# Kernel optimization log

Measured on AMD Instinct MI355X. Metric: run time of the kernel, lower is better.

Reference implementation:

```python
import jax, jax.numpy as jnp
import numpy as np

CTX = 64       # context_size_samples
HOP = 128      # stft hop
CUT = 129      # filter_length//2 + 1


def conv1d(x, w, b, stride, pad):
    # x: [B, Cin, L], w: [Cout, Cin, K]
    out = jax.lax.conv_general_dilated(
        x, w, window_strides=(stride,), padding=[(pad, pad)],
        dimension_numbers=("NCH", "OIH", "NCH"))
    return out + b[None, :, None]


def setup_inputs() -> dict:
    key = jax.random.key(0)
    ks = jax.random.split(key, 16)
    B = 32768
    s = 0.05  # small init scale to avoid gate/sigmoid saturation
    inp = {
        "x": jax.random.normal(ks[0], (B, 512), jnp.float32),
        "h0": jnp.zeros((B, 128), jnp.float32),
        "c0": jnp.zeros((B, 128), jnp.float32),
        "basis": jax.random.normal(ks[1], (258, 1, 256), jnp.float32) * s,
        "w1": jax.random.normal(ks[2], (128, 129, 3), jnp.float32) * s,
        "b1": jax.random.normal(ks[3], (128,), jnp.float32) * s,
        "w2": jax.random.normal(ks[4], (64, 128, 3), jnp.float32) * s,
        "b2": jax.random.normal(ks[5], (64,), jnp.float32) * s,
        "w3": jax.random.normal(ks[6], (64, 64, 3), jnp.float32) * s,
        "b3": jax.random.normal(ks[7], (64,), jnp.float32) * s,
        "w4": jax.random.normal(ks[8], (128, 64, 3), jnp.float32) * s,
        "b4": jax.random.normal(ks[9], (128,), jnp.float32) * s,
        "w_ih": jax.random.normal(ks[10], (512, 128), jnp.float32) * s,
        "w_hh": jax.random.normal(ks[11], (512, 128), jnp.float32) * s,
        "b_ih": jax.random.normal(ks[12], (512,), jnp.float32) * s,
        "b_hh": jax.random.normal(ks[13], (512,), jnp.float32) * s,
        "dec_w": jax.random.normal(ks[14], (1, 128, 1), jnp.float32) * s,
        "dec_b": jax.random.normal(ks[15], (1,), jnp.float32) * s,
    }
    return inp


def reference(x, h0, c0, basis, w1, b1, w2, b2, w3, b3, w4, b4,
              w_ih, w_hh, b_ih, b_hh, dec_w, dec_b):
    B = x.shape[0]
    # prepend zero context, reflect-pad by 64 (ConvSTFT)
    xc = jnp.concatenate([jnp.zeros((B, CTX), x.dtype), x], axis=1)  # [B,576]
    xp = jnp.pad(xc, ((0, 0), (64, 64)), mode="reflect")[:, None, :]  # [B,1,704]
    ft = jax.lax.conv_general_dilated(
        xp, basis, window_strides=(HOP,), padding=[(0, 0)],
        dimension_numbers=("NCH", "OIH", "NCH"))  # [B,258,4]
    real, imag = ft[:, :CUT, :], ft[:, CUT:, :]
    mag = jnp.sqrt(real * real + imag * imag)  # [B,129,4]
    # encoder: 4 conv+relu blocks
    e = jax.nn.relu(conv1d(mag, w1, b1, 1, 1))   # [B,128,4]
    e = jax.nn.relu(conv1d(e, w2, b2, 2, 1))     # [B,64,2]
    e = jax.nn.relu(conv1d(e, w3, b3, 2, 1))     # [B,64,1]
    e = jax.nn.relu(conv1d(e, w4, b4, 1, 1))     # [B,128,1]
    dec_in = e[:, :, 0]  # [B,128]
    # LSTM cell (gate order i,f,g,o as in the slicing)
    gates = dec_in @ w_ih.T + b_ih + h0 @ w_hh.T + b_hh  # [B,512]
    i, f, g, o = jnp.split(gates, 4, axis=1)
    c1 = jax.nn.sigmoid(f) * c0 + jax.nn.sigmoid(i) * jnp.tanh(g)
    h1 = jax.nn.sigmoid(o) * jnp.tanh(c1)
    # decoder: (eval-mode dropout = identity) -> ReLU -> 1x1 conv -> sigmoid
    out = jax.nn.sigmoid(jax.nn.relu(h1) @ dec_w[0, :, 0] + dec_b[0])  # [B]
    # mean over length-1 dim + squeeze is identity here
    return out, h1, c1
```

## Files before the change

### kernel.cpp

```cpp
#include <hip/hip_runtime.h>

typedef _Float16 f16;
typedef _Float16 f16x8 __attribute__((ext_vector_type(8)));
typedef _Float16 f16x4 __attribute__((ext_vector_type(4)));
typedef float f32x4 __attribute__((ext_vector_type(4)));

#define MFMA16(a, b, c) __builtin_amdgcn_mfma_f32_16x16x32_f16((a), (b), (c), 0, 0, 0)

#define BATCH 32768

#define OFF_XP      ((size_t)0)
#define OFF_MAGP    ((size_t)46137344)
#define OFF_BF      (OFF_MAGP + 54525952)
#define OFF_W1      (OFF_BF + 139264)
#define OFF_W2      (OFF_W1 + 106496)
#define OFF_W3      (OFF_W2 + 49152)
#define OFF_W4      (OFF_W3 + 24576)
#define OFF_WG      (OFF_W4 + 16384)

__device__ __forceinline__ float sigmoid_(float x) { return 1.f / (1.f + __expf(-x)); }

__global__ __launch_bounds__(256) void prep_kernel(
    const float* __restrict__ x, const float* __restrict__ basis,
    const float* __restrict__ w1, const float* __restrict__ w2,
    const float* __restrict__ w3, const float* __restrict__ w4,
    const float* __restrict__ w_ih, const float* __restrict__ w_hh,
    f16* __restrict__ xp, f16* __restrict__ magP,
    f16* __restrict__ Bf3, f16* __restrict__ W1i, f16* __restrict__ W2,
    f16* __restrict__ W3, f16* __restrict__ W4, f16* __restrict__ Wg) {
  int blk = blockIdx.x;
  int tid = threadIdx.x;
  if (blk < 1024) {
    int b0 = blk * 32;
    for (int idx = tid; idx < 32 * 176; idx += 256) {
      int bl = idx / 176, g = idx - bl * 176;
      int b = b0 + bl;
      f16x4 o;
      if (g < 32) {
        float v0 = (g == 0) ? x[(size_t)b * 512] : 0.f;
        o = (f16x4){(f16)v0, (f16)0.f, (f16)0.f, (f16)0.f};
      } else if (g < 160) {
        const float4 v = *(const float4*)(x + (size_t)b * 512 + 4 * g - 128);
        o = (f16x4){(f16)v.x, (f16)v.y, (f16)v.z, (f16)v.w};
      } else {
        int j0 = 4 * g;
        const float* xb = x + (size_t)b * 512;
        o = (f16x4){(f16)xb[1150 - j0], (f16)xb[1149 - j0], (f16)xb[1148 - j0],
                    (f16)xb[1147 - j0]};
      }
      *(f16x4*)(xp + (size_t)b * 704 + 4 * g) = o;
    }
    f16x8 z8 = {};
    for (int idx = tid; idx < 32 * 36; idx += 256) {
      int bl = idx / 36, g = idx - bl * 36;
      int off = (g < 17) ? g * 8 : 680 + (g - 17) * 8;
      *(f16x8*)(magP + (size_t)(b0 + bl) * 832 + off) = z8;
    }
  } else {
    int t = (blk - 1024) * 256 + tid;
    for (int idx = t; idx < 8 * 17 * 512; idx += 16384) {
      int jj = idx & 7;
      int lane = (idx >> 3) & 63;
      int rest = idx >> 9;
      int tt = rest % 17, kb = rest / 17;
      int n = tt * 16 + (lane & 15);
      int k = kb * 32 + (lane >> 4) * 8 + jj;
      Bf3[idx] = (f16)((n < 258) ? basis[n * 256 + k] : 0.f);
    }
    for (int idx = t; idx < 13 * 128 * 32; idx += 16384) {
      int kb = idx / 4096, rest = idx - kb * 4096;
      int n = rest >> 5, kk = rest & 31;
      int k = kb * 32 + kk;
      int tap = k / 136, i = k - tap * 136;
      float v = (tap < 3 && i < 129) ? w1[(n * 129 + i) * 3 + tap] : 0.f;
      W1i[idx] = (f16)v;
    }
    for (int idx = t; idx < 64 * 384; idx += 16384) {
      int n = idx / 384, k = idx - n * 384;
      int tap = k >> 7, i = k & 127;
      W2[idx] = (f16)w2[(n * 128 + i) * 3 + tap];
    }
    for (int idx = t; idx < 64 * 192; idx += 16384) {
      int n = idx / 192, k = idx - n * 192;
      int tap = k >> 6, i = k & 63;
      W3[idx] = (f16)w3[(n * 64 + i) * 3 + tap];
    }
    for (int idx = t; idx < 128 * 64; idx += 16384) {
      int n = idx >> 6, i = idx & 63;
      W4[idx] = (f16)w4[(n * 64 + i) * 3 + 1];
    }
    for (int idx = t; idx < 512 * 256; idx += 16384) {
      int n = idx >> 8, k = idx & 255;
      Wg[idx] = (f16)((k < 128) ? w_ih[n * 128 + k] : w_hh[n * 128 + (k - 128)]);
    }
  }
}

__global__ __launch_bounds__(256) void stft_kernel(
    const f16* __restrict__ xp, const f16* __restrict__ Bf3,
    f16* __restrict__ magP) {
  __shared__ __align__(16) f16 Bslab[2][17 * 512];
  __shared__ float imPatch[4][64];
  int tid = threadIdx.x;
  int lane = tid & 63, wv = tid >> 6;
  int l15 = lane & 15, quad = lane >> 4;
  int m0 = blockIdx.x * 64;

  int t0 = 2 * wv, t1 = 2 * wv + 1, t2 = 2 * wv + 8, t3 = 2 * wv + 9;

  f32x4 zero4 = {0.f, 0.f, 0.f, 0.f};
  f32x4 acc[4][4];
  f32x4 acc4[4];
#pragma unroll
  for (int s = 0; s < 4; s++)
#pragma unroll
    for (int mt = 0; mt < 4; mt++) acc[s][mt] = zero4;
#pragma unroll
  for (int mt = 0; mt < 4; mt++) acc4[mt] = zero4;

  const f16* aptr[4];
#pragma unroll
  for (int mt = 0; mt < 4; mt++) {
    int m = m0 + mt * 16 + l15;
    int b = m >> 2, t = m & 3;
    aptr[mt] = xp + (size_t)b * 704 + t * 128 + quad * 8;
  }

  f16x8 stg[5];
#pragma unroll
  for (int i = 0; i < 5; i++) {
    int j = wv + 4 * i;
    if (j < 17) stg[i] = *(const f16x8*)(Bf3 + (size_t)j * 512 + lane * 8);
  }
#pragma unroll
  for (int i = 0; i < 5; i++) {
    int j = wv + 4 * i;
    if (j < 17) *(f16x8*)&Bslab[0][j * 512 + lane * 8] = stg[i];
  }

  for (int kb = 0; kb < 8; kb++) {
    __syncthreads();
    int cur = kb & 1;
    if (kb < 7) {
#pragma unroll
      for (int i = 0; i < 5; i++) {
        int j = wv + 4 * i;
        if (j < 17)
          stg[i] = *(const f16x8*)(Bf3 + ((size_t)(kb + 1) * 17 + j) * 512 +
                                   lane * 8);
      }
    }
    f16x8 a[4];
#pragma unroll
    for (int mt = 0; mt < 4; mt++) a[mt] = *(const f16x8*)(aptr[mt] + kb * 32);
    {
      f16x8 b0f = *(const f16x8*)&Bslab[cur][t0 * 512 + lane * 8];
      f16x8 b1f = *(const f16x8*)&Bslab[cur][t1 * 512 + lane * 8];
      f16x8 b2f = *(const f16x8*)&Bslab[cur][t2 * 512 + lane * 8];
      f16x8 b3f = *(const f16x8*)&Bslab[cur][t3 * 512 + lane * 8];
#pragma unroll
      for (int mt = 0; mt < 4; mt++) {
        acc[0][mt] = MFMA16(a[mt], b0f, acc[0][mt]);
        acc[1][mt] = MFMA16(a[mt], b1f, acc[1][mt]);
        acc[2][mt] = MFMA16(a[mt], b2f, acc[2][mt]);
        acc[3][mt] = MFMA16(a[mt], b3f, acc[3][mt]);
      }
      if (wv == 0) {
        f16x8 b4f = *(const f16x8*)&Bslab[cur][16 * 512 + lane * 8];
#pragma unroll
        for (int mt = 0; mt < 4; mt++) acc4[mt] = MFMA16(a[mt], b4f, acc4[mt]);
      }
    }
    if (kb < 7) {
#pragma unroll
      for (int i = 0; i < 5; i++) {
        int j = wv + 4 * i;
        if (j < 17) *(f16x8*)&Bslab[cur ^ 1][j * 512 + lane * 8] = stg[i];
      }
    }
  }

  __syncthreads();
  {
    int dst = (wv == 0) ? 3 : (wv - 1);
    if (l15 == 0) {
#pragma unroll
      for (int mt = 0; mt < 4; mt++)
#pragma unroll
        for (int r = 0; r < 4; r++) {
          int row = mt * 16 + quad * 4 + r;
          imPatch[dst][row] = (wv == 0) ? acc4[mt][r] : acc[2][mt][r];
        }
    }
  }
  __syncthreads();

#pragma unroll
  for (int mt = 0; mt < 4; mt++)
#pragma unroll
    for (int r = 0; r < 4; r++) {
      int row = mt * 16 + quad * 4 + r;
      int m = m0 + row;
      int b = m >> 2, t = m & 3;
      f16* orow = magP + (size_t)b * 832 + (t + 1) * 136;
      {
        float re = acc[0][mt][r];
        float imA = __shfl(acc[2][mt][r], (quad << 4) | ((l15 + 1) & 15), 64);
        float imB = __shfl(acc[3][mt][r], quad << 4, 64);
        float im = (l15 == 15) ? imB : imA;
        orow[32 * wv + l15] = (f16)sqrtf(re * re + im * im);
      }
      {
        float re = acc[1][mt][r];
        float imA = __shfl(acc[3][mt][r], (quad << 4) | ((l15 + 1) & 15), 64);
        float im = (l15 == 15) ? imPatch[wv][row] : imA;
        orow[32 * wv + 16 + l15] = (f16)sqrtf(re * re + im * im);
      }
      if (wv == 0) {
        float re = acc[2][mt][r];
        float im = __shfl(acc4[mt][r], (quad << 4) | 1, 64);
        if (l15 == 0) orow[128] = (f16)sqrtf(re * re + im * im);
      }
    }
}

__global__ __launch_bounds__(256) void tail_kernel(
    const f16* __restrict__ magP, const f16* __restrict__ W1i,
    const float* __restrict__ b1, const f16* __restrict__ W2,
    const float* __restrict__ b2, const f16* __restrict__ W3,
    const float* __restrict__ b3, const f16* __restrict__ W4,
    const float* __restrict__ b4, const f16* __restrict__ Wg,
    const float* __restrict__ b_ih, const float* __restrict__ b_hh,
    const float* __restrict__ h0, const float* __restrict__ c0,
    const float* __restrict__ dec_w, const float* __restrict__ dec_b,
    float* __restrict__ out) {
  __shared__ __align__(16) char smem[54272];
  f16* SF = (f16*)smem;
  float* part = (float*)(smem + 21504);
#define E1(bl, s, c) ((bl) * 648 + (s) * 128 + (c))
#define E2(bl, s, c) (20736 + (bl) * 200 + (s) * 64 + (c))
#define E3(bl, c) ((bl) * 72 + (c))
#define E4(bl, k) (2304 + (bl) * 264 + (k))

  int tid = threadIdx.x;
  int lane = tid & 63, wv = tid >> 6;
  int l15 = lane & 15, quad = lane >> 4;
  int b0 = blockIdx.x * 32;
  f32x4 zero4 = {0.f, 0.f, 0.f, 0.f};

  {
    f16x8 z8 = {};
    for (int idx = tid; idx < 512; idx += 256) {
      int bl = idx >> 4, g = idx & 15;
      *(f16x8*)&SF[E1(bl, 0, g * 8)] = z8;
    }
    for (int idx = tid; idx < 256; idx += 256) {
      int bl = idx >> 3, g = idx & 7;
      *(f16x8*)&SF[E2(bl, 0, g * 8)] = z8;
    }
  }

  {
    f32x4 acc1[8][2];
#pragma unroll
    for (int mt = 0; mt < 8; mt++)
#pragma unroll
      for (int nt = 0; nt < 2; nt++) acc1[mt][nt] = zero4;
    const f16* aptr[8];
#pragma unroll
    for (int mt = 0; mt < 8; mt++) {
      int row = mt * 16 + l15;
      int b = b0 + (row >> 2), p = row & 3;
      aptr[mt] = magP + (size_t)b * 832 + p * 136 + quad * 8;
    }
    const f16* bbase = W1i + ((2 * wv) * 16 + l15) * 32 + quad * 8;
    for (int kb = 0; kb < 13; kb++) {
      f16x8 a[8];
#pragma unroll
      for (int mt = 0; mt < 8; mt++) a[mt] = *(const f16x8*)(aptr[mt] + kb * 32);
      f16x8 bf0 = *(const f16x8*)(bbase + kb * 4096);
      f16x8 bf1 = *(const f16x8*)(bbase + kb * 4096 + 512);
#pragma unroll
      for (int mt = 0; mt < 8; mt++) {
        acc1[mt][0] = MFMA16(a[mt], bf0, acc1[mt][0]);
        acc1[mt][1] = MFMA16(a[mt], bf1, acc1[mt][1]);
      }
    }
    float bias[2];
#pragma unroll
    for (int nt = 0; nt < 2; nt++) bias[nt] = b1[(2 * wv + nt) * 16 + l15];
#pragma unroll
    for (int mt = 0; mt < 8; mt++)
#pragma unroll
      for (int r = 0; r < 4; r++) {
        int row = mt * 16 + quad * 4 + r;
        int bl = row >> 2, p = row & 3;
#pragma unroll
        for (int nt = 0; nt < 2; nt++) {
          int c = (2 * wv + nt) * 16 + l15;
          SF[E1(bl, p + 1, c)] = (f16)fmaxf(acc1[mt][nt][r] + bias[nt], 0.f);
        }
      }
  }
  __syncthreads();

  {
    int wr = wv & 1, wc = wv >> 1;
    f32x4 acc2[2][2];
#pragma unroll
    for (int mt = 0; mt < 2; mt++)
#pragma unroll
      for (int nt = 0; nt < 2; nt++) acc2[mt][nt] = zero4;
    int abase[2];
#pragma unroll
    for (int mt = 0; mt < 2; mt++) {
      int row2 = wr * 32 + mt * 16 + l15;
      int bl = row2 >> 1, p2 = row2 & 1;
      abase[mt] = E1(bl, 2 * p2, quad * 8);
    }
    const f16* bbase = W2 + (size_t)(wc * 32 + l15) * 384 + quad * 8;
    for (int kb = 0; kb < 12; kb++) {
      f16x8 a0 = *(const f16x8*)&SF[abase[0] + kb * 32];
      f16x8 a1 = *(const f16x8*)&SF[abase[1] + kb * 32];
      f16x8 bf0 = *(const f16x8*)(bbase + kb * 32);
      f16x8 bf1 = *(const f16x8*)(bbase + 16 * 384 + kb * 32);
      acc2[0][0] = MFMA16(a0, bf0, acc2[0][0]);
      acc2[1][0] = MFMA16(a1, bf0, acc2[1][0]);
      acc2[0][1] = MFMA16(a0, bf1, acc2[0][1]);
      acc2[1][1] = MFMA16(a1, bf1, acc2[1][1]);
    }
    float bias[2];
#pragma unroll
    for (int nt = 0; nt < 2; nt++) bias[nt] = b2[wc * 32 + nt * 16 + l15];
#pragma unroll
    for (int mt = 0; mt < 2; mt++)
#pragma unroll
      for (int r = 0; r < 4; r++) {
        int row2 = wr * 32 + mt * 16 + quad * 4 + r;
        int bl = row2 >> 1, p2 = row2 & 1;
#pragma unroll
        for (int nt = 0; nt < 2; nt++) {
          int c = wc * 32 + nt * 16 + l15;
          SF[E2(bl, p2 + 1, c)] = (f16)fmaxf(acc2[mt][nt][r] + bias[nt], 0.f);
        }
      }
  }
  __syncthreads();

  {
    for (int idx = tid; idx < 1024; idx += 256) {
      int bl = idx >> 5, jg = idx & 31;
      const float4 v = *(const float4*)(h0 + (size_t)(b0 + bl) * 128 + jg * 4);
      f16x4 o = {(f16)v.x, (f16)v.y, (f16)v.z, (f16)v.w};
      *(f16x4*)&SF[E4(bl, 128 + jg * 4)] = o;
    }
    f32x4 acc3[2];
#pragma unroll
    for (int mt = 0; mt < 2; mt++) acc3[mt] = zero4;
    const f16* bbase = W3 + (size_t)(wv * 16 + l15) * 192 + quad * 8;
    for (int kb = 0; kb < 6; kb++) {
      f16x8 a0 = *(const f16x8*)&SF[E2(l15, 0, 0) + kb * 32 + quad * 8];
      f16x8 a1 = *(const f16x8*)&SF[E2(16 + l15, 0, 0) + kb * 32 + quad * 8];
      f16x8 bf = *(const f16x8*)(bbase + kb * 32);
      acc3[0] = MFMA16(a0, bf, acc3[0]);
      acc3[1] = MFMA16(a1, bf, acc3[1]);
    }
    float bias = b3[wv * 16 + l15];
#pragma unroll
    for (int mt = 0; mt < 2; mt++)
#pragma unroll
      for (int r = 0; r < 4; r++) {
        int bl = mt * 16 + quad * 4 + r;
        SF[E3(bl, wv * 16 + l15)] = (f16)fmaxf(acc3[mt][r] + bias, 0.f);
      }
  }
  __syncthreads();

  {
    f32x4 acc4[2][2];
#pragma unroll
    for (int mt = 0; mt < 2; mt++)
#pragma unroll
      for (int nt = 0; nt < 2; nt++) acc4[mt][nt] = zero4;
    const f16* bbase = W4 + (size_t)(wv * 32 + l15) * 64 + quad * 8;
    for (int kb = 0; kb < 2; kb++) {
      f16x8 a0 = *(const f16x8*)&SF[E3(l15, kb * 32 + quad * 8)];
      f16x8 a1 = *(const f16x8*)&SF[E3(16 + l15, kb * 32 + quad * 8)];
      f16x8 bf0 = *(const f16x8*)(bbase + kb * 32);
      f16x8 bf1 = *(const f16x8*)(bbase + 16 * 64 + kb * 32);
      acc4[0][0] = MFMA16(a0, bf0, acc4[0][0]);
      acc4[1][0] = MFMA16(a1, bf0, acc4[1][0]);
      acc4[0][1] = MFMA16(a0, bf1, acc4[0][1]);
      acc4[1][1] = MFMA16(a1, bf1, acc4[1][1]);
    }
    float bias[2];
#pragma unroll
    for (int nt = 0; nt < 2; nt++) bias[nt] = b4[wv * 32 + nt * 16 + l15];
#pragma unroll
    for (int mt = 0; mt < 2; mt++)
#pragma unroll
      for (int r = 0; r < 4; r++) {
        int bl = mt * 16 + quad * 4 + r;
#pragma unroll
        for (int nt = 0; nt < 2; nt++) {
          int c = wv * 32 + nt * 16 + l15;
          SF[E4(bl, c)] = (f16)fmaxf(acc4[mt][nt][r] + bias[nt], 0.f);
        }
      }
  }
  __syncthreads();

  {
    f32x4 accg[8][2];
#pragma unroll
    for (int j = 0; j < 8; j++)
#pragma unroll
      for (int mt = 0; mt < 2; mt++) accg[j][mt] = zero4;
    const f16* bptrs[8];
#pragma unroll
    for (int q = 0; q < 4; q++)
#pragma unroll
      for (int u = 0; u < 2; u++)
        bptrs[q * 2 + u] =
            Wg + (size_t)(q * 128 + wv * 32 + u * 16 + l15) * 256 + quad * 8;
    for (int kb = 0; kb < 8; kb++) {
      f16x8 a0 = *(const f16x8*)&SF[E4(l15, kb * 32 + quad * 8)];
      f16x8 a1 = *(const f16x8*)&SF[E4(16 + l15, kb * 32 + quad * 8)];
#pragma unroll
      for (int j = 0; j < 8; j++) {
        f16x8 bf = *(const f16x8*)(bptrs[j] + kb * 32);
        accg[j][0] = MFMA16(a0, bf, accg[j][0]);
        accg[j][1] = MFMA16(a1, bf, accg[j][1]);
      }
    }
    float bias[8], dw[2];
#pragma unroll
    for (int q = 0; q < 4; q++)
#pragma unroll
      for (int u = 0; u < 2; u++) {
        int n = q * 128 + wv * 32 + u * 16 + l15;
        bias[q * 2 + u] = b_ih[n] + b_hh[n];
      }
#pragma unroll
    for (int u = 0; u < 2; u++) dw[u] = dec_w[wv * 32 + u * 16 + l15];

    float* out_h1 = out + BATCH;
    float* out_c1 = out + BATCH + (size_t)BATCH * 128;
#pragma unroll
    for (int mt = 0; mt < 2; mt++)
#pragma unroll
      for (int r = 0; r < 4; r++) {
        int bl = mt * 16 + quad * 4 + r;
        int b = b0 + bl;
        float p = 0.f;
#pragma unroll
        for (int u = 0; u < 2; u++) {
          int c = wv * 32 + u * 16 + l15;
          float iv = accg[0 + u][mt][r] + bias[0 + u];
          float fv = accg[2 + u][mt][r] + bias[2 + u];
          float gv = accg[4 + u][mt][r] + bias[4 + u];
          float ov = accg[6 + u][mt][r] + bias[6 + u];
          float c0v = c0[(size_t)b * 128 + c];
          float c1 = sigmoid_(fv) * c0v + sigmoid_(iv) * tanhf(gv);
          float h1 = sigmoid_(ov) * tanhf(c1);
          out_h1[(size_t)b * 128 + c] = h1;
          out_c1[(size_t)b * 128 + c] = c1;
          p += fmaxf(h1, 0.f) * dw[u];
        }
        p += __shfl_xor(p, 1);
        p += __shfl_xor(p, 2);
        p += __shfl_xor(p, 4);
        p += __shfl_xor(p, 8);
        if (l15 == 0) part[wv * 32 + bl] = p;
      }
  }
  __syncthreads();
  if (tid < 32) {
    float s = part[tid] + part[32 + tid] + part[64 + tid] + part[96 + tid] +
              dec_b[0];
    out[b0 + tid] = 1.f / (1.f + __expf(-s));
  }
#undef E1
#undef E2
#undef E3
#undef E4
}

extern "C" void kernel_launch(void* const* d_in, const int* in_sizes, int n_in,
                              void* d_out, int out_size, void* d_ws,
                              size_t ws_size, hipStream_t stream) {
  const float* x = (const float*)d_in[0];
  const float* h0 = (const float*)d_in[1];
  const float* c0 = (const float*)d_in[2];
  const float* basis = (const float*)d_in[3];
  const float* w1 = (const float*)d_in[4];
  const float* b1 = (const float*)d_in[5];
  const float* w2 = (const float*)d_in[6];
  const float* b2 = (const float*)d_in[7];
  const float* w3 = (const float*)d_in[8];
  const float* b3 = (const float*)d_in[9];
  const float* w4 = (const float*)d_in[10];
  const float* b4 = (const float*)d_in[11];
  const float* w_ih = (const float*)d_in[12];
  const float* w_hh = (const float*)d_in[13];
  const float* b_ih = (const float*)d_in[14];
  const float* b_hh = (const float*)d_in[15];
  const float* dec_w = (const float*)d_in[16];
  const float* dec_b = (const float*)d_in[17];

  char* ws = (char*)d_ws;
  f16* xp = (f16*)(ws + OFF_XP);
  f16* magP = (f16*)(ws + OFF_MAGP);
  f16* Bf3 = (f16*)(ws + OFF_BF);
  f16* W1i = (f16*)(ws + OFF_W1);
  f16* W2 = (f16*)(ws + OFF_W2);
  f16* W3 = (f16*)(ws + OFF_W3);
  f16* W4 = (f16*)(ws + OFF_W4);
  f16* Wg = (f16*)(ws + OFF_WG);

  prep_kernel<<<1088, 256, 0, stream>>>(x, basis, w1, w2, w3, w4, w_ih, w_hh,
                                        xp, magP, Bf3, W1i, W2, W3, W4, Wg);
  stft_kernel<<<2048, 256, 0, stream>>>(xp, Bf3, magP);
  tail_kernel<<<1024, 256, 0, stream>>>(magP, W1i, b1, W2, b2, W3, b3, W4, b4,
                                        Wg, b_ih, b_hh, h0, c0, dec_w, dec_b,
                                        (float*)d_out);
}
```

Before: 359.1 us.

## Fuse STFT and encoder convs into one kernel, split LSTM gates out

Padding the input, the STFT matmul, the magnitude and all four encoder conv layers now run in one kernel per 16-sample tile, with intermediates held in shared memory. This removes the global round trips through the padded-input and magnitude buffers. Only the encoder output, plus h0 written by the prep kernel, goes to a small global buffer, and a separate gates kernel runs the LSTM matmul on 64-row tiles. In exchange, the basis and conv weights are read straight from global or cache into registers rather than staged in LDS, tiles are smaller (16 rows), and the kernel uses more LDS per block.

```diff
diff --git a/kernel.cpp b/kernel.cpp
--- a/kernel.cpp
+++ b/kernel.cpp
@@ -9,9 +9,8 @@
 
 #define BATCH 32768
 
-#define OFF_XP      ((size_t)0)
-#define OFF_MAGP    ((size_t)46137344)
-#define OFF_BF      (OFF_MAGP + 54525952)
+#define OFF_GATESA  ((size_t)0)
+#define OFF_BF      (OFF_GATESA + 16777216)
 #define OFF_W1      (OFF_BF + 139264)
 #define OFF_W2      (OFF_W1 + 106496)
 #define OFF_W3      (OFF_W2 + 49152)
@@ -21,40 +20,22 @@
 __device__ __forceinline__ float sigmoid_(float x) { return 1.f / (1.f + __expf(-x)); }
 
 __global__ __launch_bounds__(256) void prep_kernel(
-    const float* __restrict__ x, const float* __restrict__ basis,
+    const float* __restrict__ h0, const float* __restrict__ basis,
     const float* __restrict__ w1, const float* __restrict__ w2,
     const float* __restrict__ w3, const float* __restrict__ w4,
     const float* __restrict__ w_ih, const float* __restrict__ w_hh,
-    f16* __restrict__ xp, f16* __restrict__ magP,
-    f16* __restrict__ Bf3, f16* __restrict__ W1i, f16* __restrict__ W2,
-    f16* __restrict__ W3, f16* __restrict__ W4, f16* __restrict__ Wg) {
+    f16* __restrict__ gatesA, f16* __restrict__ Bf3, f16* __restrict__ W1i,
+    f16* __restrict__ W2, f16* __restrict__ W3, f16* __restrict__ W4,
+    f16* __restrict__ Wg) {
   int blk = blockIdx.x;
   int tid = threadIdx.x;
   if (blk < 1024) {
     int b0 = blk * 32;
-    for (int idx = tid; idx < 32 * 176; idx += 256) {
-      int bl = idx / 176, g = idx - bl * 176;
-      int b = b0 + bl;
-      f16x4 o;
-      if (g < 32) {
-        float v0 = (g == 0) ? x[(size_t)b * 512] : 0.f;
-        o = (f16x4){(f16)v0, (f16)0.f, (f16)0.f, (f16)0.f};
-      } else if (g < 160) {
-        const float4 v = *(const float4*)(x + (size_t)b * 512 + 4 * g - 128);
-        o = (f16x4){(f16)v.x, (f16)v.y, (f16)v.z, (f16)v.w};
-      } else {
-        int j0 = 4 * g;
-        const float* xb = x + (size_t)b * 512;
-        o = (f16x4){(f16)xb[1150 - j0], (f16)xb[1149 - j0], (f16)xb[1148 - j0],
-                    (f16)xb[1147 - j0]};
-      }
-      *(f16x4*)(xp + (size_t)b * 704 + 4 * g) = o;
-    }
-    f16x8 z8 = {};
-    for (int idx = tid; idx < 32 * 36; idx += 256) {
-      int bl = idx / 36, g = idx - bl * 36;
-      int off = (g < 17) ? g * 8 : 680 + (g - 17) * 8;
-      *(f16x8*)(magP + (size_t)(b0 + bl) * 832 + off) = z8;
+    for (int idx = tid; idx < 32 * 32; idx += 256) {
+      int bl = idx >> 5, g = idx & 31;
+      const float4 v = *(const float4*)(h0 + (size_t)(b0 + bl) * 128 + g * 4);
+      f16x4 o = {(f16)v.x, (f16)v.y, (f16)v.z, (f16)v.w};
+      *(f16x4*)(gatesA + (size_t)(b0 + bl) * 256 + 128 + g * 4) = o;
     }
   } else {
     int t = (blk - 1024) * 256 + tid;
@@ -96,394 +77,362 @@
   }
 }
 
-__global__ __launch_bounds__(256) void stft_kernel(
-    const f16* __restrict__ xp, const f16* __restrict__ Bf3,
-    f16* __restrict__ magP) {
-  __shared__ __align__(16) f16 Bslab[2][17 * 512];
-  __shared__ float imPatch[4][64];
+__global__ __launch_bounds__(256, 2) void fused_kernel(
+    const float* __restrict__ x, const f16* __restrict__ Bf3,
+    const f16* __restrict__ W1i, const float* __restrict__ b1,
+    const f16* __restrict__ W2, const float* __restrict__ b2,
+    const f16* __restrict__ W3, const float* __restrict__ b3,
+    const f16* __restrict__ W4, const float* __restrict__ b4,
+    f16* __restrict__ gatesA) {
+  __shared__ __align__(16) char smem[57088];
+  f16* SF = (f16*)smem;
+  float* imPatch = (float*)(smem + 56064);
+#define XP(bl, j) ((bl)*712 + (j))
+#define E1(bl, s, c) ((bl)*648 + (s)*128 + (c))
+#define E3(bl, c) ((bl)*72 + (c))
+#define MG(bl, j) (11392 + (bl)*840 + (j))
+#define E2(bl, s, c) (24832 + (bl)*200 + (s)*64 + (c))
+
   int tid = threadIdx.x;
   int lane = tid & 63, wv = tid >> 6;
   int l15 = lane & 15, quad = lane >> 4;
-  int m0 = blockIdx.x * 64;
-
-  int t0 = 2 * wv, t1 = 2 * wv + 1, t2 = 2 * wv + 8, t3 = 2 * wv + 9;
-
+  int b0 = blockIdx.x * 16;
   f32x4 zero4 = {0.f, 0.f, 0.f, 0.f};
-  f32x4 acc[4][4];
-  f32x4 acc4[4];
-#pragma unroll
-  for (int s = 0; s < 4; s++)
-#pragma unroll
-    for (int mt = 0; mt < 4; mt++) acc[s][mt] = zero4;
-#pragma unroll
-  for (int mt = 0; mt < 4; mt++) acc4[mt] = zero4;
-
-  const f16* aptr[4];
-#pragma unroll
-  for (int mt = 0; mt < 4; mt++) {
-    int m = m0 + mt * 16 + l15;
-    int b = m >> 2, t = m & 3;
-    aptr[mt] = xp + (size_t)b * 704 + t * 128 + quad * 8;
-  }
-
-  f16x8 stg[5];
-#pragma unroll
-  for (int i = 0; i < 5; i++) {
-    int j = wv + 4 * i;
-    if (j < 17) stg[i] = *(const f16x8*)(Bf3 + (size_t)j * 512 + lane * 8);
-  }
-#pragma unroll
-  for (int i = 0; i < 5; i++) {
-    int j = wv + 4 * i;
-    if (j < 17) *(f16x8*)&Bslab[0][j * 512 + lane * 8] = stg[i];
-  }
-
-  for (int kb = 0; kb < 8; kb++) {
+
+  for (int idx = tid; idx < 16 * 176; idx += 256) {
+    int bl = idx / 176, g = idx - bl * 176;
+    int b = b0 + bl;
+    f16x4 o;
+    if (g < 32) {
+      float v0 = (g == 0) ? x[(size_t)b * 512] : 0.f;
+      o = (f16x4){(f16)v0, (f16)0.f, (f16)0.f, (f16)0.f};
+    } else if (g < 160) {
+      const float4 v = *(const float4*)(x + (size_t)b * 512 + 4 * g - 128);
+      o = (f16x4){(f16)v.x, (f16)v.y, (f16)v.z, (f16)v.w};
+    } else {
+      int j0 = 4 * g;
+      const float* xb = x + (size_t)b * 512;
+      o = (f16x4){(f16)xb[1150 - j0], (f16)xb[1149 - j0], (f16)xb[1148 - j0],
+                  (f16)xb[1147 - j0]};
+    }
+    *(f16x4*)&SF[XP(bl, 4 * g)] = o;
+  }
+  {
+    f16x8 z8 = {};
+    for (int idx = tid; idx < 16 * 105; idx += 256) {
+      int bl = idx / 105, g = idx - bl * 105;
+      *(f16x8*)&SF[MG(bl, g * 8)] = z8;
+    }
+    for (int idx = tid; idx < 16 * 8; idx += 256) {
+      int bl = idx >> 3, g = idx & 7;
+      *(f16x8*)&SF[E2(bl, 0, g * 8)] = z8;
+    }
+  }
+  __syncthreads();
+
+  {
+    int t0 = 2 * wv, t1 = t0 + 1, t2 = t0 + 8, t3 = t0 + 9;
+    f32x4 acc[4][4];
+    f32x4 acc4[4];
+#pragma unroll
+    for (int s = 0; s < 4; s++)
+#pragma unroll
+      for (int mt = 0; mt < 4; mt++) acc[s][mt] = zero4;
+#pragma unroll
+    for (int mt = 0; mt < 4; mt++) acc4[mt] = zero4;
+
+    const f16* Bl = Bf3 + lane * 8;
+    f16x8 bc0 = *(const f16x8*)(Bl + t0 * 512);
+    f16x8 bc1 = *(const f16x8*)(Bl + t1 * 512);
+    f16x8 bc2 = *(const f16x8*)(Bl + t2 * 512);
+    f16x8 bc3 = *(const f16x8*)(Bl + t3 * 512);
+    f16x8 bc4 = {};
+    if (wv == 0) bc4 = *(const f16x8*)(Bl + 16 * 512);
+
+    for (int kb = 0; kb < 8; kb++) {
+      f16x8 bn0, bn1, bn2, bn3, bn4;
+      if (kb < 7) {
+        const f16* Bn = Bl + (size_t)(kb + 1) * 17 * 512;
+        bn0 = *(const f16x8*)(Bn + t0 * 512);
+        bn1 = *(const f16x8*)(Bn + t1 * 512);
+        bn2 = *(const f16x8*)(Bn + t2 * 512);
+        bn3 = *(const f16x8*)(Bn + t3 * 512);
+        if (wv == 0) bn4 = *(const f16x8*)(Bn + 16 * 512);
+      }
+      f16x8 a[4];
+#pragma unroll
+      for (int mt = 0; mt < 4; mt++)
+        a[mt] = *(const f16x8*)&SF[XP(l15, mt * 128 + kb * 32 + quad * 8)];
+#pragma unroll
+      for (int mt = 0; mt < 4; mt++) {
+        acc[0][mt] = MFMA16(a[mt], bc0, acc[0][mt]);
+        acc[1][mt] = MFMA16(a[mt], bc1, acc[1][mt]);
+        acc[2][mt] = MFMA16(a[mt], bc2, acc[2][mt]);
+        acc[3][mt] = MFMA16(a[mt], bc3, acc[3][mt]);
+      }
+      if (wv == 0) {
+#pragma unroll
+        for (int mt = 0; mt < 4; mt++) acc4[mt] = MFMA16(a[mt], bc4, acc4[mt]);
+      }
+      if (kb < 7) {
+        bc0 = bn0; bc1 = bn1; bc2 = bn2; bc3 = bn3;
+        if (wv == 0) bc4 = bn4;
+      }
+    }
+
+    {
+      int dst = (wv == 0) ? 3 : (wv - 1);
+      if (l15 == 0) {
+#pragma unroll
+        for (int mt = 0; mt < 4; mt++)
+#pragma unroll
+          for (int r = 0; r < 4; r++) {
+            int row = mt * 16 + quad * 4 + r;
+            imPatch[dst * 64 + row] = (wv == 0) ? acc4[mt][r] : acc[2][mt][r];
+          }
+      }
+    }
     __syncthreads();
-    int cur = kb & 1;
-    if (kb < 7) {
-#pragma unroll
-      for (int i = 0; i < 5; i++) {
-        int j = wv + 4 * i;
-        if (j < 17)
-          stg[i] = *(const f16x8*)(Bf3 + ((size_t)(kb + 1) * 17 + j) * 512 +
-                                   lane * 8);
-      }
-    }
-    f16x8 a[4];
-#pragma unroll
-    for (int mt = 0; mt < 4; mt++) a[mt] = *(const f16x8*)(aptr[mt] + kb * 32);
-    {
-      f16x8 b0f = *(const f16x8*)&Bslab[cur][t0 * 512 + lane * 8];
-      f16x8 b1f = *(const f16x8*)&Bslab[cur][t1 * 512 + lane * 8];
-      f16x8 b2f = *(const f16x8*)&Bslab[cur][t2 * 512 + lane * 8];
-      f16x8 b3f = *(const f16x8*)&Bslab[cur][t3 * 512 + lane * 8];
-#pragma unroll
-      for (int mt = 0; mt < 4; mt++) {
-        acc[0][mt] = MFMA16(a[mt], b0f, acc[0][mt]);
-        acc[1][mt] = MFMA16(a[mt], b1f, acc[1][mt]);
-        acc[2][mt] = MFMA16(a[mt], b2f, acc[2][mt]);
-        acc[3][mt] = MFMA16(a[mt], b3f, acc[3][mt]);
-      }
-      if (wv == 0) {
-        f16x8 b4f = *(const f16x8*)&Bslab[cur][16 * 512 + lane * 8];
-#pragma unroll
-        for (int mt = 0; mt < 4; mt++) acc4[mt] = MFMA16(a[mt], b4f, acc4[mt]);
-      }
-    }
-    if (kb < 7) {
-#pragma unroll
-      for (int i = 0; i < 5; i++) {
-        int j = wv + 4 * i;
-        if (j < 17) *(f16x8*)&Bslab[cur ^ 1][j * 512 + lane * 8] = stg[i];
-      }
-    }
-  }
-
-  __syncthreads();
-  {
-    int dst = (wv == 0) ? 3 : (wv - 1);
-    if (l15 == 0) {
-#pragma unroll
-      for (int mt = 0; mt < 4; mt++)
-#pragma unroll
-        for (int r = 0; r < 4; r++) {
+
+#pragma unroll
+    for (int mt = 0; mt < 4; mt++)
+#pragma unroll
+      for (int r = 0; r < 4; r++) {
+        int bl = quad * 4 + r;
+        int orow = MG(bl, (mt + 1) * 136);
+        {
+          float re = acc[0][mt][r];
+          float imA = __shfl(acc[2][mt][r], (quad << 4) | ((l15 + 1) & 15), 64);
+          float imB = __shfl(acc[3][mt][r], quad << 4, 64);
+          float im = (l15 == 15) ? imB : imA;
+          SF[orow + 32 * wv + l15] = (f16)sqrtf(re * re + im * im);
+        }
+        {
+          float re = acc[1][mt][r];
+          float imA = __shfl(acc[3][mt][r], (quad << 4) | ((l15 + 1) & 15), 64);
           int row = mt * 16 + quad * 4 + r;
-          imPatch[dst][row] = (wv == 0) ? acc4[mt][r] : acc[2][mt][r];
+          float im = (l15 == 15) ? imPatch[wv * 64 + row] : imA;
+          SF[orow + 32 * wv + 16 + l15] = (f16)sqrtf(re * re + im * im);
         }
-    }
-  }
-  __syncthreads();
-
-#pragma unroll
-  for (int mt = 0; mt < 4; mt++)
+        if (wv == 0) {
+          float re = acc[2][mt][r];
+          float im = __shfl(acc4[mt][r], (quad << 4) | 1, 64);
+          if (l15 == 0) SF[orow + 128] = (f16)sqrtf(re * re + im * im);
+        }
+      }
+  }
+  __syncthreads();
+
+  {
+    f16x8 z8 = {};
+    for (int idx = tid; idx < 16 * 16; idx += 256) {
+      int bl = idx >> 4, g = idx & 15;
+      *(f16x8*)&SF[E1(bl, 0, g * 8)] = z8;
+    }
+    f32x4 acc1[4][2];
+#pragma unroll
+    for (int p = 0; p < 4; p++)
+#pragma unroll
+      for (int nt = 0; nt < 2; nt++) acc1[p][nt] = zero4;
+    const f16* bbase = W1i + ((2 * wv) * 16 + l15) * 32 + quad * 8;
+    f16x8 bc0 = *(const f16x8*)(bbase);
+    f16x8 bc1 = *(const f16x8*)(bbase + 512);
+    for (int kb = 0; kb < 13; kb++) {
+      f16x8 bn0, bn1;
+      if (kb < 12) {
+        bn0 = *(const f16x8*)(bbase + (kb + 1) * 4096);
+        bn1 = *(const f16x8*)(bbase + (kb + 1) * 4096 + 512);
+      }
+      f16x8 a[4];
+#pragma unroll
+      for (int p = 0; p < 4; p++)
+        a[p] = *(const f16x8*)&SF[MG(l15, p * 136 + kb * 32 + quad * 8)];
+#pragma unroll
+      for (int p = 0; p < 4; p++) {
+        acc1[p][0] = MFMA16(a[p], bc0, acc1[p][0]);
+        acc1[p][1] = MFMA16(a[p], bc1, acc1[p][1]);
+      }
+      if (kb < 12) { bc0 = bn0; bc1 = bn1; }
+    }
+    float bias[2];
+#pragma unroll
+    for (int nt = 0; nt < 2; nt++) bias[nt] = b1[(2 * wv + nt) * 16 + l15];
+#pragma unroll
+    for (int p = 0; p < 4; p++)
+#pragma unroll
+      for (int r = 0; r < 4; r++) {
+        int bl = quad * 4 + r;
+#pragma unroll
+        for (int nt = 0; nt < 2; nt++) {
+          int c = (2 * wv + nt) * 16 + l15;
+          SF[E1(bl, p + 1, c)] = (f16)fmaxf(acc1[p][nt][r] + bias[nt], 0.f);
+        }
+      }
+  }
+  __syncthreads();
+
+  {
+    int wr = wv & 1, wc = wv >> 1;
+    f32x4 acc2[2] = {zero4, zero4};
+    const f16* bbase = W2 + (size_t)(wc * 32 + l15) * 384 + quad * 8;
+    f16x8 bc0 = *(const f16x8*)(bbase);
+    f16x8 bc1 = *(const f16x8*)(bbase + 16 * 384);
+    for (int kb = 0; kb < 12; kb++) {
+      f16x8 bn0, bn1;
+      if (kb < 11) {
+        bn0 = *(const f16x8*)(bbase + (kb + 1) * 32);
+        bn1 = *(const f16x8*)(bbase + 16 * 384 + (kb + 1) * 32);
+      }
+      f16x8 a = *(const f16x8*)&SF[E1(l15, wr * 2, kb * 32 + quad * 8)];
+      acc2[0] = MFMA16(a, bc0, acc2[0]);
+      acc2[1] = MFMA16(a, bc1, acc2[1]);
+      if (kb < 11) { bc0 = bn0; bc1 = bn1; }
+    }
+    float bias[2] = {b2[wc * 32 + l15], b2[wc * 32 + 16 + l15]};
 #pragma unroll
     for (int r = 0; r < 4; r++) {
-      int row = mt * 16 + quad * 4 + r;
-      int m = m0 + row;
-      int b = m >> 2, t = m & 3;
-      f16* orow = magP + (size_t)b * 832 + (t + 1) * 136;
-      {
-        float re = acc[0][mt][r];
-        float imA = __shfl(acc[2][mt][r], (quad << 4) | ((l15 + 1) & 15), 64);
-        float imB = __shfl(acc[3][mt][r], quad << 4, 64);
-        float im = (l15 == 15) ? imB : imA;
-        orow[32 * wv + l15] = (f16)sqrtf(re * re + im * im);
-      }
-      {
-        float re = acc[1][mt][r];
-        float imA = __shfl(acc[3][mt][r], (quad << 4) | ((l15 + 1) & 15), 64);
-        float im = (l15 == 15) ? imPatch[wv][row] : imA;
-        orow[32 * wv + 16 + l15] = (f16)sqrtf(re * re + im * im);
-      }
-      if (wv == 0) {
-        float re = acc[2][mt][r];
-        float im = __shfl(acc4[mt][r], (quad << 4) | 1, 64);
-        if (l15 == 0) orow[128] = (f16)sqrtf(re * re + im * im);
-      }
-    }
+      int bl = quad * 4 + r;
+      SF[E2(bl, wr + 1, wc * 32 + l15)] = (f16)fmaxf(acc2[0][r] + bias[0], 0.f);
+      SF[E2(bl, wr + 1, wc * 32 + 16 + l15)] =
+          (f16)fmaxf(acc2[1][r] + bias[1], 0.f);
+    }
+  }
+  __syncthreads();
+
+  {
+    f32x4 acc3 = zero4;
+    const f16* bbase = W3 + (size_t)(wv * 16 + l15) * 192 + quad * 8;
+    for (int kb = 0; kb < 6; kb++) {
+      f16x8 a = *(const f16x8*)&SF[E2(l15, 0, kb * 32 + quad * 8)];
+      f16x8 bf = *(const f16x8*)(bbase + kb * 32);
+      acc3 = MFMA16(a, bf, acc3);
+    }
+    float bias = b3[wv * 16 + l15];
+#pragma unroll
+    for (int r = 0; r < 4; r++) {
+      int bl = quad * 4 + r;
+      SF[E3(bl, wv * 16 + l15)] = (f16)fmaxf(acc3[r] + bias, 0.f);
+    }
+  }
+  __syncthreads();
+
+  {
+    f32x4 acc4a[2] = {zero4, zero4};
+    const f16* bbase = W4 + (size_t)(wv * 32 + l15) * 64 + quad * 8;
+    for (int kb = 0; kb < 2; kb++) {
+      f16x8 a = *(const f16x8*)&SF[E3(l15, kb * 32 + quad * 8)];
+      f16x8 bf0 = *(const f16x8*)(bbase + kb * 32);
+      f16x8 bf1 = *(const f16x8*)(bbase + 16 * 64 + kb * 32);
+      acc4a[0] = MFMA16(a, bf0, acc4a[0]);
+      acc4a[1] = MFMA16(a, bf1, acc4a[1]);
+    }
+    float bias[2] = {b4[wv * 32 + l15], b4[wv * 32 + 16 + l15]};
+#pragma unroll
+    for (int r = 0; r < 4; r++) {
+      int bl = quad * 4 + r;
+      gatesA[(size_t)(b0 + bl) * 256 + wv * 32 + l15] =
+          (f16)fmaxf(acc4a[0][r] + bias[0], 0.f);
+      gatesA[(size_t)(b0 + bl) * 256 + wv * 32 + 16 + l15] =
+          (f16)fmaxf(acc4a[1][r] + bias[1], 0.f);
+    }
+  }
+#undef XP
+#undef MG
+#undef E1
+#undef E2
+#undef E3
 }
 
-__global__ __launch_bounds__(256) void tail_kernel(
-    const f16* __restrict__ magP, const f16* __restrict__ W1i,
-    const float* __restrict__ b1, const f16* __restrict__ W2,
-    const float* __restrict__ b2, const f16* __restrict__ W3,
-    const float* __restrict__ b3, const f16* __restrict__ W4,
-    const float* __restrict__ b4, const f16* __restrict__ Wg,
+__global__ __launch_bounds__(256) void gates_kernel(
+    const f16* __restrict__ gatesA, const f16* __restrict__ Wg,
     const float* __restrict__ b_ih, const float* __restrict__ b_hh,
-    const float* __restrict__ h0, const float* __restrict__ c0,
-    const float* __restrict__ dec_w, const float* __restrict__ dec_b,
-    float* __restrict__ out) {
-  __shared__ __align__(16) char smem[54272];
-  f16* SF = (f16*)smem;
-  float* part = (float*)(smem + 21504);
-#define E1(bl, s, c) ((bl) * 648 + (s) * 128 + (c))
-#define E2(bl, s, c) (20736 + (bl) * 200 + (s) * 64 + (c))
-#define E3(bl, c) ((bl) * 72 + (c))
-#define E4(bl, k) (2304 + (bl) * 264 + (k))
-
+    const float* __restrict__ c0, const float* __restrict__ dec_w,
+    const float* __restrict__ dec_b, float* __restrict__ out) {
+  __shared__ float part[4][64];
   int tid = threadIdx.x;
   int lane = tid & 63, wv = tid >> 6;
   int l15 = lane & 15, quad = lane >> 4;
-  int b0 = blockIdx.x * 32;
+  int b0 = blockIdx.x * 64;
   f32x4 zero4 = {0.f, 0.f, 0.f, 0.f};
 
-  {
-    f16x8 z8 = {};
-    for (int idx = tid; idx < 512; idx += 256) {
-      int bl = idx >> 4, g = idx & 15;
-      *(f16x8*)&SF[E1(bl, 0, g * 8)] = z8;
-    }
-    for (int idx = tid; idx < 256; idx += 256) {
-      int bl = idx >> 3, g = idx & 7;
-      *(f16x8*)&SF[E2(bl, 0, g * 8)] = z8;
-    }
-  }
-
-  {
-    f32x4 acc1[8][2];
-#pragma unroll
-    for (int mt = 0; mt < 8; mt++)
-#pragma unroll
-      for (int nt = 0; nt < 2; nt++) acc1[mt][nt] = zero4;
-    const f16* aptr[8];
-#pragma unroll
-    for (int mt = 0; mt < 8; mt++) {
-      int row = mt * 16 + l15;
-      int b = b0 + (row >> 2), p = row & 3;
-      aptr[mt] = magP + (size_t)b * 832 + p * 136 + quad * 8;
-    }
-    const f16* bbase = W1i + ((2 * wv) * 16 + l15) * 32 + quad * 8;
-    for (int kb = 0; kb < 13; kb++) {
-      f16x8 a[8];
-#pragma unroll
-      for (int mt = 0; mt < 8; mt++) a[mt] = *(const f16x8*)(aptr[mt] + kb * 32);
-      f16x8 bf0 = *(const f16x8*)(bbase + kb * 4096);
-      f16x8 bf1 = *(const f16x8*)(bbase + kb * 4096 + 512);
-#pragma unroll
-      for (int mt = 0; mt < 8; mt++) {
-        acc1[mt][0] = MFMA16(a[mt], bf0, acc1[mt][0]);
-        acc1[mt][1] = MFMA16(a[mt], bf1, acc1[mt][1]);
-      }
-    }
-    float bias[2];
-#pragma unroll
-    for (int nt = 0; nt < 2; nt++) bias[nt] = b1[(2 * wv + nt) * 16 + l15];
-#pragma unroll
-    for (int mt = 0; mt < 8; mt++)
-#pragma unroll
-      for (int r = 0; r < 4; r++) {
-        int row = mt * 16 + quad * 4 + r;
-        int bl = row >> 2, p = row & 3;
-#pragma unroll
-        for (int nt = 0; nt < 2; nt++) {
-          int c = (2 * wv + nt) * 16 + l15;
-          SF[E1(bl, p + 1, c)] = (f16)fmaxf(acc1[mt][nt][r] + bias[nt], 0.f);
-        }
-      }
-  }
-  __syncthreads();
-
-  {
-    int wr = wv & 1, wc = wv >> 1;
-    f32x4 acc2[2][2];
-#pragma unroll
-    for (int mt = 0; mt < 2; mt++)
-#pragma unroll
-      for (int nt = 0; nt < 2; nt++) acc2[mt][nt] = zero4;
-    int abase[2];
-#pragma unroll
-    for (int mt = 0; mt < 2; mt++) {
-      int row2 = wr * 32 + mt * 16 + l15;
-      int bl = row2 >> 1, p2 = row2 & 1;
-      abase[mt] = E1(bl, 2 * p2, quad * 8);
-    }
-    const f16* bbase = W2 + (size_t)(wc * 32 + l15) * 384 + quad * 8;
-    for (int kb = 0; kb < 12; kb++) {
-      f16x8 a0 = *(const f16x8*)&SF[abase[0] + kb * 32];
-      f16x8 a1 = *(const f16x8*)&SF[abase[1] + kb * 32];
-      f16x8 bf0 = *(const f16x8*)(bbase + kb * 32);
-      f16x8 bf1 = *(const f16x8*)(bbase + 16 * 384 + kb * 32);
-      acc2[0][0] = MFMA16(a0, bf0, acc2[0][0]);
-      acc2[1][0] = MFMA16(a1, bf0, acc2[1][0]);
-      acc2[0][1] = MFMA16(a0, bf1, acc2[0][1]);
-      acc2[1][1] = MFMA16(a1, bf1, acc2[1][1]);
-    }
-    float bias[2];
-#pragma unroll
-    for (int nt = 0; nt < 2; nt++) bias[nt] = b2[wc * 32 + nt * 16 + l15];
-#pragma unroll
-    for (int mt = 0; mt < 2; mt++)
-#pragma unroll
-      for (int r = 0; r < 4; r++) {
-        int row2 = wr * 32 + mt * 16 + quad * 4 + r;
-        int bl = row2 >> 1, p2 = row2 & 1;
-#pragma unroll
-        for (int nt = 0; nt < 2; nt++) {
-          int c = wc * 32 + nt * 16 + l15;
-          SF[E2(bl, p2 + 1, c)] = (f16)fmaxf(acc2[mt][nt][r] + bias[nt], 0.f);
-        }
-      }
-  }
-  __syncthreads();
-
-  {
-    for (int idx = tid; idx < 1024; idx += 256) {
-      int bl = idx >> 5, jg = idx & 31;
-      const float4 v = *(const float4*)(h0 + (size_t)(b0 + bl) * 128 + jg * 4);
-      f16x4 o = {(f16)v.x, (f16)v.y, (f16)v.z, (f16)v.w};
-      *(f16x4*)&SF[E4(bl, 128 + jg * 4)] = o;
-    }
-    f32x4 acc3[2];
-#pragma unroll
-    for (int mt = 0; mt < 2; mt++) acc3[mt] = zero4;
-    const f16* bbase = W3 + (size_t)(wv * 16 + l15) * 192 + quad * 8;
-    for (int kb = 0; kb < 6; kb++) {
-      f16x8 a0 = *(const f16x8*)&SF[E2(l15, 0, 0) + kb * 32 + quad * 8];
-      f16x8 a1 = *(const f16x8*)&SF[E2(16 + l15, 0, 0) + kb * 32 + quad * 8];
-      f16x8 bf = *(const f16x8*)(bbase + kb * 32);
-      acc3[0] = MFMA16(a0, bf, acc3[0]);
-      acc3[1] = MFMA16(a1, bf, acc3[1]);
-    }
-    float bias = b3[wv * 16 + l15];
-#pragma unroll
-    for (int mt = 0; mt < 2; mt++)
-#pragma unroll
-      for (int r = 0; r < 4; r++) {
-        int bl = mt * 16 + quad * 4 + r;
-        SF[E3(bl, wv * 16 + l15)] = (f16)fmaxf(acc3[mt][r] + bias, 0.f);
-      }
-  }
-  __syncthreads();
-
-  {
-    f32x4 acc4[2][2];
-#pragma unroll
-    for (int mt = 0; mt < 2; mt++)
-#pragma unroll
-      for (int nt = 0; nt < 2; nt++) acc4[mt][nt] = zero4;
-    const f16* bbase = W4 + (size_t)(wv * 32 + l15) * 64 + quad * 8;
-    for (int kb = 0; kb < 2; kb++) {
-      f16x8 a0 = *(const f16x8*)&SF[E3(l15, kb * 32 + quad * 8)];
-      f16x8 a1 = *(const f16x8*)&SF[E3(16 + l15, kb * 32 + quad * 8)];
-      f16x8 bf0 = *(const f16x8*)(bbase + kb * 32);
-      f16x8 bf1 = *(const f16x8*)(bbase + 16 * 64 + kb * 32);
-      acc4[0][0] = MFMA16(a0, bf0, acc4[0][0]);
-      acc4[1][0] = MFMA16(a1, bf0, acc4[1][0]);
-      acc4[0][1] = MFMA16(a0, bf1, acc4[0][1]);
-      acc4[1][1] = MFMA16(a1, bf1, acc4[1][1]);
-    }
-    float bias[2];
-#pragma unroll
-    for (int nt = 0; nt < 2; nt++) bias[nt] = b4[wv * 32 + nt * 16 + l15];
-#pragma unroll
-    for (int mt = 0; mt < 2; mt++)
-#pragma unroll
-      for (int r = 0; r < 4; r++) {
-        int bl = mt * 16 + quad * 4 + r;
-#pragma unroll
-        for (int nt = 0; nt < 2; nt++) {
-          int c = wv * 32 + nt * 16 + l15;
-          SF[E4(bl, c)] = (f16)fmaxf(acc4[mt][nt][r] + bias[nt], 0.f);
-        }
-      }
-  }
-  __syncthreads();
-
-  {
-    f32x4 accg[8][2];
-#pragma unroll
-    for (int j = 0; j < 8; j++)
-#pragma unroll
-      for (int mt = 0; mt < 2; mt++) accg[j][mt] = zero4;
-    const f16* bptrs[8];
-#pragma unroll
-    for (int q = 0; q < 4; q++)
-#pragma unroll
-      for (int u = 0; u < 2; u++)
-        bptrs[q * 2 + u] =
-            Wg + (size_t)(q * 128 + wv * 32 + u * 16 + l15) * 256 + quad * 8;
-    for (int kb = 0; kb < 8; kb++) {
-      f16x8 a0 = *(const f16x8*)&SF[E4(l15, kb * 32 + quad * 8)];
-      f16x8 a1 = *(const f16x8*)&SF[E4(16 + l15, kb * 32 + quad * 8)];
-#pragma unroll
-      for (int j = 0; j < 8; j++) {
-        f16x8 bf = *(const f16x8*)(bptrs[j] + kb * 32);
-        accg[j][0] = MFMA16(a0, bf, accg[j][0]);
-        accg[j][1] = MFMA16(a1, bf, accg[j][1]);
-      }
-    }
-    float bias[8], dw[2];
-#pragma unroll
-    for (int q = 0; q < 4; q++)
+  float* out_h1 = out + BATCH;
+  float* out_c1 = out + BATCH + (size_t)BATCH * 128;
+
+  f32x4 acc[4][8];
+#pragma unroll
+  for (int mt = 0; mt < 4; mt++)
+#pragma unroll
+    for (int j = 0; j < 8; j++) acc[mt][j] = zero4;
+
+  const f16* aptr[4];
+#pragma unroll
+  for (int mt = 0; mt < 4; mt++)
+    aptr[mt] = gatesA + (size_t)(b0 + mt * 16 + l15) * 256 + quad * 8;
+
+  const f16* bptrs[8];
+#pragma unroll
+  for (int q = 0; q < 4; q++)
+#pragma unroll
+    for (int u = 0; u < 2; u++)
+      bptrs[q * 2 + u] =
+          Wg + (size_t)(q * 128 + wv * 32 + u * 16 + l15) * 256 + quad * 8;
+
+  for (int k0 = 0; k0 < 256; k0 += 32) {
+    f16x8 a[4];
+#pragma unroll
+    for (int mt = 0; mt < 4; mt++) a[mt] = *(const f16x8*)(aptr[mt] + k0);
+#pragma unroll
+    for (int j = 0; j < 8; j++) {
+      f16x8 bf = *(const f16x8*)(bptrs[j] + k0);
+#pragma unroll
+      for (int mt = 0; mt < 4; mt++) acc[mt][j] = MFMA16(a[mt], bf, acc[mt][j]);
+    }
+  }
+
+  float bias[8], dw[2];
+#pragma unroll
+  for (int q = 0; q < 4; q++)
+#pragma unroll
+    for (int u = 0; u < 2; u++) {
+      int n = q * 128 + wv * 32 + u * 16 + l15;
+      bias[q * 2 + u] = b_ih[n] + b_hh[n];
+    }
+#pragma unroll
+  for (int u = 0; u < 2; u++) dw[u] = dec_w[wv * 32 + u * 16 + l15];
+
+#pragma unroll
+  for (int mt = 0; mt < 4; mt++)
+#pragma unroll
+    for (int r = 0; r < 4; r++) {
+      int bl = mt * 16 + quad * 4 + r;
+      int b = b0 + bl;
+      float p = 0.f;
 #pragma unroll
       for (int u = 0; u < 2; u++) {
-        int n = q * 128 + wv * 32 + u * 16 + l15;
-        bias[q * 2 + u] = b_ih[n] + b_hh[n];
-      }
-#pragma unroll
-    for (int u = 0; u < 2; u++) dw[u] = dec_w[wv * 32 + u * 16 + l15];
-
-    float* out_h1 = out + BATCH;
-    float* out_c1 = out + BATCH + (size_t)BATCH * 128;
-#pragma unroll
-    for (int mt = 0; mt < 2; mt++)
-#pragma unroll
-      for (int r = 0; r < 4; r++) {
-        int bl = mt * 16 + quad * 4 + r;
-        int b = b0 + bl;
-        float p = 0.f;
-#pragma unroll
-        for (int u = 0; u < 2; u++) {
-          int c = wv * 32 + u * 16 + l15;
-          float iv = accg[0 + u][mt][r] + bias[0 + u];
-          float fv = accg[2 + u][mt][r] + bias[2 + u];
-          float gv = accg[4 + u][mt][r] + bias[4 + u];
-          float ov = accg[6 + u][mt][r] + bias[6 + u];
-          float c0v = c0[(size_t)b * 128 + c];
-          float c1 = sigmoid_(fv) * c0v + sigmoid_(iv) * tanhf(gv);
-          float h1 = sigmoid_(ov) * tanhf(c1);
-          out_h1[(size_t)b * 128 + c] = h1;
-          out_c1[(size_t)b * 128 + c] = c1;
-          p += fmaxf(h1, 0.f) * dw[u];
-        }
-        p += __shfl_xor(p, 1);
-        p += __shfl_xor(p, 2);
-        p += __shfl_xor(p, 4);
-        p += __shfl_xor(p, 8);
-        if (l15 == 0) part[wv * 32 + bl] = p;
-      }
-  }
-  __syncthreads();
-  if (tid < 32) {
-    float s = part[tid] + part[32 + tid] + part[64 + tid] + part[96 + tid] +
+        int c = wv * 32 + u * 16 + l15;
+        float iv = acc[mt][0 + u][r] + bias[0 + u];
+        float fv = acc[mt][2 + u][r] + bias[2 + u];
+        float gv = acc[mt][4 + u][r] + bias[4 + u];
+        float ov = acc[mt][6 + u][r] + bias[6 + u];
+        float c0v = c0[(size_t)b * 128 + c];
+        float c1 = sigmoid_(fv) * c0v + sigmoid_(iv) * tanhf(gv);
+        float h1 = sigmoid_(ov) * tanhf(c1);
+        out_h1[(size_t)b * 128 + c] = h1;
+        out_c1[(size_t)b * 128 + c] = c1;
+        p += fmaxf(h1, 0.f) * dw[u];
+      }
+      p += __shfl_xor(p, 1);
+      p += __shfl_xor(p, 2);
+      p += __shfl_xor(p, 4);
+      p += __shfl_xor(p, 8);
+      if (l15 == 0) part[wv][bl] = p;
+    }
+  __syncthreads();
+  if (tid < 64) {
+    float s = part[0][tid] + part[1][tid] + part[2][tid] + part[3][tid] +
               dec_b[0];
     out[b0 + tid] = 1.f / (1.f + __expf(-s));
   }
-#undef E1
-#undef E2
-#undef E3
-#undef E4
 }
 
 extern "C" void kernel_launch(void* const* d_in, const int* in_sizes, int n_in,
@@ -509,8 +458,7 @@
   const float* dec_b = (const float*)d_in[17];
 
   char* ws = (char*)d_ws;
-  f16* xp = (f16*)(ws + OFF_XP);
-  f16* magP = (f16*)(ws + OFF_MAGP);
+  f16* gatesA = (f16*)(ws + OFF_GATESA);
   f16* Bf3 = (f16*)(ws + OFF_BF);
   f16* W1i = (f16*)(ws + OFF_W1);
   f16* W2 = (f16*)(ws + OFF_W2);
@@ -518,10 +466,10 @@
   f16* W4 = (f16*)(ws + OFF_W4);
   f16* Wg = (f16*)(ws + OFF_WG);
 
-  prep_kernel<<<1088, 256, 0, stream>>>(x, basis, w1, w2, w3, w4, w_ih, w_hh,
-                                        xp, magP, Bf3, W1i, W2, W3, W4, Wg);
-  stft_kernel<<<2048, 256, 0, stream>>>(xp, Bf3, magP);
-  tail_kernel<<<1024, 256, 0, stream>>>(magP, W1i, b1, W2, b2, W3, b3, W4, b4,
-                                        Wg, b_ih, b_hh, h0, c0, dec_w, dec_b,
-                                        (float*)d_out);
+  prep_kernel<<<1088, 256, 0, stream>>>(h0, basis, w1, w2, w3, w4, w_ih, w_hh,
+                                        gatesA, Bf3, W1i, W2, W3, W4, Wg);
+  fused_kernel<<<2048, 256, 0, stream>>>(x, Bf3, W1i, b1, W2, b2, W3, b3, W4,
+                                         b4, gatesA);
+  gates_kernel<<<512, 256, 0, stream>>>(gatesA, Wg, b_ih, b_hh, c0, dec_w,
+                                        dec_b, (float*)d_out);
 }
```

After: 327.3 us. 1.1x faster.
